# Kernel tuning notes

Measured on AMD Instinct MI355X. Metric: run time of the kernel, lower is better.

## Reference

```python
import jax, jax.numpy as jnp
import numpy as np

N = 4096
M = 1024
APPERTURE = 250
L1, L2, L3, PRED = 1024, 512, 128, 1
EPS = 1e-6


def _layer_norm(x, gamma, beta):
    # torch x.std(-1) is unbiased (ddof=1)
    mean = jnp.mean(x, axis=-1, keepdims=True)
    std = jnp.std(x, axis=-1, ddof=1, keepdims=True)
    return gamma * (x - mean) / (std + EPS) + beta


def _self_attention(x, Wq, Wk, Wv, Wo, band_mask):
    # x: [n, m]; Linear(bias=False) => x @ W.T
    K = x @ Wk.T
    Q = (x @ Wq.T) * 0.06
    V = x @ Wv.T
    logits = Q @ K.T                      # [n, n]
    logits = jnp.where(band_mask, logits, -jnp.inf)  # keep |i-j| < apperture
    att = jax.nn.softmax(logits, axis=-1)
    # original: y = (V^T @ att)^T == att^T @ V  (note the transpose!)
    y = att.T @ V
    return y @ Wo.T, att


def setup_inputs() -> dict:
    key = jax.random.key(0)
    ks = jax.random.split(key, 20)
    s = 0.02
    inp = {
        'x1': jax.random.normal(ks[0], (1, N, M), jnp.float32),
        'x2': jax.random.normal(ks[1], (1, N, M), jnp.float32),
        'x3': jax.random.normal(ks[2], (1, N, M), jnp.float32),
        'Wq': jax.random.normal(ks[3], (M, M), jnp.float32) * s,
        'Wk': jax.random.normal(ks[4], (M, M), jnp.float32) * s,
        'Wv': jax.random.normal(ks[5], (M, M), jnp.float32) * s,
        'Wo': jax.random.normal(ks[6], (M, M), jnp.float32) * s,
        'ka_w': jax.random.normal(ks[7], (L1, M), jnp.float32) * s,
        'ka_b': jnp.zeros((L1,), jnp.float32),
        'kb_w': jax.random.normal(ks[8], (L2, L1), jnp.float32) * s,
        'kb_b': jnp.zeros((L2,), jnp.float32),
        'kc_w': jax.random.normal(ks[9], (L3, L2), jnp.float32) * s,
        'kc_b': jnp.zeros((L3,), jnp.float32),
        'kd_w': jax.random.normal(ks[10], (PRED, L3), jnp.float32) * s,
        'kd_b': jnp.zeros((PRED,), jnp.float32),
        'g13': jnp.ones((M,), jnp.float32),
        'b13': jnp.zeros((M,), jnp.float32),
        'gkc': jnp.ones((L3,), jnp.float32),
        'bkc': jnp.zeros((L3,), jnp.float32),
        'seq_len': N,
    }
    return inp


def reference(x1, x2, x3, Wq, Wk, Wv, Wo, ka_w, ka_b, kb_w, kb_b, kc_w, kc_b,
              kd_w, kd_b, g13, b13, gkc, bkc, seq_len):
    x1 = x1.reshape(-1, x1.shape[2])
    x2 = x2.reshape(-1, x2.shape[2])
    x3 = x3.reshape(-1, x3.shape[2])
    n = x1.shape[0]
    idx = jnp.arange(n)
    band_mask = jnp.abs(idx[:, None] - idx[None, :]) < APPERTURE  # allowed

    y1, att1 = _self_attention(x1, Wq, Wk, Wv, Wo, band_mask)
    y2, _ = _self_attention(x2, Wq, Wk, Wv, Wo, band_mask)
    y3, _ = _self_attention(x3, Wq, Wk, Wv, Wo, band_mask)

    # residual + (dropout == identity in eval) + shared LayerNorm
    y1 = _layer_norm(y1 + x1, g13, b13)
    y2 = _layer_norm(y2 + x2, g13, b13)
    y3 = _layer_norm(y3 + x3, g13, b13)

    y = y1 + y2 + y3  # cmb == [1,1,1]
    y = y @ ka_w.T + ka_b
    y = y @ kb_w.T + kb_b
    y = jax.nn.relu(y @ kc_w.T + kc_b)
    y = _layer_norm(y, gkc, bkc)
    y = jax.nn.sigmoid(y @ kd_w.T + kd_b)
    return y.reshape(1, -1), att1
```

## Files before the change

kernel.cpp:

```cpp
#include <hip/hip_runtime.h>
#include <hip/hip_bf16.h>
#include <cstdint>
#include <cstddef>

#define NSEQ 4096
#define MDIM 1024

typedef __attribute__((ext_vector_type(8))) short short8;
typedef __attribute__((ext_vector_type(4))) float f32x4;
typedef __attribute__((ext_vector_type(2))) long long2v;
typedef __attribute__((ext_vector_type(8))) int int8v;
typedef __attribute__((ext_vector_type(4))) int int4v;

typedef const __attribute__((address_space(1))) void gvoid_t;
typedef __attribute__((address_space(3))) void lvoid_t;

__device__ __forceinline__ unsigned short f2b(float x) {
  union { float f; unsigned int u; } a; a.f = x;
  unsigned int r = (a.u + 0x7fffu + ((a.u >> 16) & 1u)) >> 16;
  return (unsigned short)r;
}
__device__ __forceinline__ float b2f(unsigned short u) {
  union { float f; unsigned int u32; } a; a.u32 = ((unsigned int)u) << 16;
  return a.f;
}
__device__ __forceinline__ unsigned char f2e4(float x) {
  return (unsigned char)(__builtin_amdgcn_cvt_pk_fp8_f32(x, x, 0, false) & 0xff);
}
__device__ __forceinline__ unsigned int f2e4x4(float a, float b, float c, float d) {
  unsigned int lo = __builtin_amdgcn_cvt_pk_fp8_f32(a, b, 0, false);
  return (unsigned int)__builtin_amdgcn_cvt_pk_fp8_f32(c, d, lo, true);
}

__device__ __forceinline__ int8v pack32(const unsigned char* p0,
                                        const unsigned char* p1) {
  int4v lo = *(const int4v*)p0;
  int4v hi = *(const int4v*)p1;
  int8v r;
  r[0] = lo[0]; r[1] = lo[1]; r[2] = lo[2]; r[3] = lo[3];
  r[4] = hi[0]; r[5] = hi[1]; r[6] = hi[2]; r[7] = hi[3];
  return r;
}

__global__ __launch_bounds__(256) void k_cvt_all(
    const float* __restrict__ s0, const float* __restrict__ s1,
    const float* __restrict__ s2, const float* __restrict__ s3,
    const float* __restrict__ s4, const float* __restrict__ s5,
    const float* __restrict__ s6,
    const float* __restrict__ xa, const float* __restrict__ xb,
    const float* __restrict__ xc,
    unsigned char* __restrict__ Wf8, unsigned short* __restrict__ Wmlp,
    unsigned char* __restrict__ Xdst) {
  int idx = blockIdx.x * 256 + threadIdx.x;
  if (idx < 1048576) {
    int seg = idx >> 18, local = idx & 262143;
    const float* src = (seg == 0) ? s0 : (seg == 1) ? s1 : (seg == 2) ? s2 : s3;
    float4 v = *(const float4*)(src + (size_t)local * 4);
    *(unsigned int*)(Wf8 + (size_t)idx * 4) =
        f2e4x4(v.x * 64.f, v.y * 64.f, v.z * 64.f, v.w * 64.f);
  } else if (idx < 1458176) {
    int i2 = idx - 1048576;
    const float* src; int local;
    if (i2 < 262144) { src = s4; local = i2; }
    else if (i2 < 393216) { src = s5; local = i2 - 262144; }
    else { src = s6; local = i2 - 393216; }
    float4 v = *(const float4*)(src + (size_t)local * 4);
    ushort4 o; o.x = f2b(v.x); o.y = f2b(v.y); o.z = f2b(v.z); o.w = f2b(v.w);
    *(ushort4*)(Wmlp + (size_t)i2 * 4) = o;
  } else {
    int i2 = idx - 1458176;
    int seg = i2 >> 20, local = i2 & 1048575;
    const float* src = (seg == 0) ? xa : (seg == 1) ? xb : xc;
    float4 v = *(const float4*)(src + (size_t)local * 4);
    *(unsigned int*)(Xdst + (size_t)i2 * 4) = f2e4x4(v.x, v.y, v.z, v.w);
  }
}

__global__ __launch_bounds__(256) void k_gemm(
    const unsigned char* __restrict__ A, int lda,
    const unsigned char* __restrict__ B, int ldb,
    void* __restrict__ Cout, void* __restrict__ Cout2, int ldc,
    int K, float alpha, int okind, int do_exp, int mode,
    const unsigned char* __restrict__ A1, const unsigned char* __restrict__ A2) {
  __shared__ unsigned char smem[4 * 128 * 128];
  int bx = blockIdx.x, by = blockIdx.y;
  const unsigned char* Ab;
  const unsigned char* Bb;
  void* Cdst = Cout;
  int k0 = 0, k1 = K, b_koff = 0;
  int ldce = ldc;
  int rbase, cbase;
  int ldae = lda, ldbe = ldb;
  if (mode == 0) {
    Ab = A + (size_t)by * 128 * lda;
    Bb = B + (size_t)bx * 128 * ldb;
    rbase = bx * 128; cbase = by * 128;
  } else if (mode == 3) {
    if (by < 16) {
      Ab = A + (size_t)by * 128 * lda;
      Bb = B + (size_t)bx * 128 * ldb;
      if (by >= 8) Cdst = Cout2;
      rbase = bx * 128; cbase = (by & 7) * 128;
    } else {
      Ab = B + (size_t)bx * 128 * ldb;
      Bb = A1 + (size_t)(by - 16) * 128 * 1024;
      Cdst = (void*)const_cast<unsigned char*>(A2);
      rbase = (by - 16) * 128; cbase = bx * 128;
      ldce = 3 * NSEQ;
    }
  } else if (mode == 1) {
    int s = bx >> 5, ti = bx & 31;
    int bt = ti + by - 2;
    if (bt < 0 || bt >= 32) return;
    Ab = A + (size_t)(s * 32 + bt) * 128 * lda;
    Bb = B + (size_t)bx * 128 * ldb;
    rbase = bx * 128; cbase = by * 128;
  } else {
    int s = bx >> 5, ti = bx & 31;
    Ab = A + (size_t)by * 128 * lda + s * NSEQ;
    const unsigned char* Bbase = (s == 0) ? B : ((s == 1) ? A1 : A2);
    Bb = Bbase + (size_t)ti * 128 * 640;
    ldbe = 640;
    int lo = ti - 2; if (lo < 0) lo = 0;
    int hi = ti + 3; if (hi > 32) hi = 32;
    k0 = lo * 128; k1 = hi * 128;
    b_koff = (ti - 2) * 128;
    rbase = bx * 128; cbase = by * 128;
  }

  const int t = threadIdx.x;
  const int l = t & 63;
  const int w = t >> 6;
  const int fr = l & 15;
  const int quad = l >> 4;
  const int wm = (w >> 1) * 64;
  const int wn = (w & 1) * 64;
  const int fq4 = quad * 4;

  int srow[4], scg[4], sloff[4];
#pragma unroll
  for (int j = 0; j < 4; j++) {
    srow[j] = w * 32 + j * 8 + (l >> 3);
    scg[j] = ((l & 7) - srow[j]) & 7;
    sloff[j] = (w * 32 + j * 8) * 128 + l * 16;
  }

  f32x4 acc[4][4];
#pragma unroll
  for (int m = 0; m < 4; m++)
#pragma unroll
    for (int n = 0; n < 4; n++) acc[m][n] = (f32x4){0.f, 0.f, 0.f, 0.f};

  const int c0 = quad * 2;
  const int nt = (k1 - k0) >> 7;

  {
    int kk = k0, kb = kk - b_koff;
#pragma unroll
    for (int j = 0; j < 4; j++)
      __builtin_amdgcn_global_load_lds(
          (gvoid_t*)(Ab + (size_t)srow[j] * ldae + kk + scg[j] * 16),
          (lvoid_t*)(smem + sloff[j]), 16, 0, 0);
#pragma unroll
    for (int j = 0; j < 4; j++)
      __builtin_amdgcn_global_load_lds(
          (gvoid_t*)(Bb + (size_t)srow[j] * ldbe + kb + scg[j] * 16),
          (lvoid_t*)(smem + 16384 + sloff[j]), 16, 0, 0);
  }

  for (int tt = 0; tt < nt; tt++) {
    __syncthreads();
    if (tt + 1 < nt) {
      int kk = k0 + (tt + 1) * 128, kb = kk - b_koff;
      unsigned char* Asn = smem + ((tt + 1) & 1) * 32768;
#pragma unroll
      for (int j = 0; j < 4; j++)
        __builtin_amdgcn_global_load_lds(
            (gvoid_t*)(Ab + (size_t)srow[j] * ldae + kk + scg[j] * 16),
            (lvoid_t*)(Asn + sloff[j]), 16, 0, 0);
#pragma unroll
      for (int j = 0; j < 4; j++)
        __builtin_amdgcn_global_load_lds(
            (gvoid_t*)(Bb + (size_t)srow[j] * ldbe + kb + scg[j] * 16),
            (lvoid_t*)(Asn + 16384 + sloff[j]), 16, 0, 0);
    }
    const unsigned char* Asc = smem + (tt & 1) * 32768;
    const unsigned char* Bsc = Asc + 16384;
    int8v a8[4], b8[4];
#pragma unroll
    for (int m = 0; m < 4; m++) {
      int r = wm + m * 16 + fr;
      int s0i = (c0 + r) & 7, s1i = (s0i + 1) & 7;
      a8[m] = pack32(Asc + r * 128 + s0i * 16, Asc + r * 128 + s1i * 16);
    }
#pragma unroll
    for (int n = 0; n < 4; n++) {
      int r = wn + n * 16 + fr;
      int s0i = (c0 + r) & 7, s1i = (s0i + 1) & 7;
      b8[n] = pack32(Bsc + r * 128 + s0i * 16, Bsc + r * 128 + s1i * 16);
    }
#pragma unroll
    for (int m = 0; m < 4; m++)
#pragma unroll
      for (int n = 0; n < 4; n++)
        acc[m][n] = __builtin_amdgcn_mfma_scale_f32_16x16x128_f8f6f4(
            a8[m], b8[n], acc[m][n], 0, 0, 0, 0x7F7F7F7F, 0, 0x7F7F7F7F);
  }

#pragma unroll
  for (int m = 0; m < 4; m++) {
#pragma unroll
    for (int n = 0; n < 4; n++) {
      int oc = cbase + wm + m * 16 + fq4;
      int orow = rbase + wn + n * 16 + fr;
      float v0 = acc[m][n][0] * alpha, v1 = acc[m][n][1] * alpha;
      float v2 = acc[m][n][2] * alpha, v3 = acc[m][n][3] * alpha;
      if (okind == 1) {
        if (do_exp) { v0 = __expf(v0); v1 = __expf(v1); v2 = __expf(v2); v3 = __expf(v3); }
        ushort4 o; o.x = f2b(v0); o.y = f2b(v1); o.z = f2b(v2); o.w = f2b(v3);
        *(uint2*)((unsigned short*)Cdst + (size_t)orow * ldce + oc) = *(uint2*)&o;
      } else if (okind == 2) {
        *(unsigned int*)((unsigned char*)Cdst + (size_t)orow * ldce + oc) =
            f2e4x4(v0, v1, v2, v3);
      } else {
        *(float4*)((float*)Cdst + (size_t)orow * ldce + oc) = make_float4(v0, v1, v2, v3);
      }
    }
  }
}

__global__ __launch_bounds__(256) void k_gemm64(
    const unsigned short* __restrict__ A, int lda,
    const unsigned short* __restrict__ B, int ldb,
    void* __restrict__ Cout, int ldc, int K,
    const float* __restrict__ bias, int relu, int out_bf16) {
  __shared__ unsigned short smem[4 * 64 * 64];
  int bx = blockIdx.x, by = blockIdx.y;
  const unsigned short* Ab = A + (size_t)by * 64 * lda;
  const unsigned short* Bb = B + (size_t)bx * 64 * ldb;
  int rbase = bx * 64, cbase = by * 64;

  const int t = threadIdx.x;
  const int l = t & 63;
  const int w = t >> 6;
  const int fr = l & 15;
  const int quad = l >> 4;
  const int wm = (w & 1) * 32;
  const int wn = (w >> 1) * 32;
  const int fq4 = quad * 4;

  int srow[2], scg[2], sloff[2];
#pragma unroll
  for (int j = 0; j < 2; j++) {
    srow[j] = w * 16 + j * 8 + (l >> 3);
    scg[j] = ((l & 7) - srow[j]) & 7;
    sloff[j] = (w * 16 + j * 8) * 64 + l * 8;
  }

  f32x4 acc[2][2];
#pragma unroll
  for (int m = 0; m < 2; m++)
#pragma unroll
    for (int n = 0; n < 2; n++) acc[m][n] = (f32x4){0.f, 0.f, 0.f, 0.f};

  const int nt = K >> 6;

#pragma unroll
  for (int j = 0; j < 2; j++)
    __builtin_amdgcn_global_load_lds(
        (gvoid_t*)(Ab + (size_t)srow[j] * lda + scg[j] * 8),
        (lvoid_t*)(smem + sloff[j]), 16, 0, 0);
#pragma unroll
  for (int j = 0; j < 2; j++)
    __builtin_amdgcn_global_load_lds(
        (gvoid_t*)(Bb + (size_t)srow[j] * ldb + scg[j] * 8),
        (lvoid_t*)(smem + 4096 + sloff[j]), 16, 0, 0);

  for (int tt = 0; tt < nt; tt++) {
    __syncthreads();
    if (tt + 1 < nt) {
      int kk = (tt + 1) * 64;
      unsigned short* Asn = smem + ((tt + 1) & 1) * 8192;
#pragma unroll
      for (int j = 0; j < 2; j++)
        __builtin_amdgcn_global_load_lds(
            (gvoid_t*)(Ab + (size_t)srow[j] * lda + kk + scg[j] * 8),
            (lvoid_t*)(Asn + sloff[j]), 16, 0, 0);
#pragma unroll
      for (int j = 0; j < 2; j++)
        __builtin_amdgcn_global_load_lds(
            (gvoid_t*)(Bb + (size_t)srow[j] * ldb + kk + scg[j] * 8),
            (lvoid_t*)(Asn + 4096 + sloff[j]), 16, 0, 0);
    }
    const unsigned short* Asc = smem + (tt & 1) * 8192;
    const unsigned short* Bsc = Asc + 4096;
#pragma unroll
    for (int s = 0; s < 2; s++) {
      short8 af[2], bf[2];
#pragma unroll
      for (int m = 0; m < 2; m++) {
        int r = wm + m * 16 + fr;
        int slot = (s * 4 + quad + r) & 7;
        af[m] = *(const short8*)(Asc + r * 64 + slot * 8);
      }
#pragma unroll
      for (int n = 0; n < 2; n++) {
        int r = wn + n * 16 + fr;
        int slot = (s * 4 + quad + r) & 7;
        bf[n] = *(const short8*)(Bsc + r * 64 + slot * 8);
      }
#pragma unroll
      for (int m = 0; m < 2; m++)
#pragma unroll
        for (int n = 0; n < 2; n++)
          acc[m][n] = __builtin_amdgcn_mfma_f32_16x16x32_bf16(af[m], bf[n], acc[m][n], 0, 0, 0);
    }
  }

#pragma unroll
  for (int m = 0; m < 2; m++) {
#pragma unroll
    for (int n = 0; n < 2; n++) {
      int oc = cbase + wm + m * 16 + fq4;
      int orow = rbase + wn + n * 16 + fr;
      float4 bv = bias ? *(const float4*)(bias + oc) : make_float4(0.f, 0.f, 0.f, 0.f);
      float v0 = acc[m][n][0] + bv.x, v1 = acc[m][n][1] + bv.y;
      float v2 = acc[m][n][2] + bv.z, v3 = acc[m][n][3] + bv.w;
      if (relu) {
        v0 = fmaxf(v0, 0.f); v1 = fmaxf(v1, 0.f);
        v2 = fmaxf(v2, 0.f); v3 = fmaxf(v3, 0.f);
      }
      if (out_bf16) {
        ushort4 o; o.x = f2b(v0); o.y = f2b(v1); o.z = f2b(v2); o.w = f2b(v3);
        *(uint2*)((unsigned short*)Cout + (size_t)orow * ldc + oc) = *(uint2*)&o;
      } else {
        *(float4*)((float*)Cout + (size_t)orow * ldc + oc) = make_float4(v0, v1, v2, v3);
      }
    }
  }
}

__global__ __launch_bounds__(256) void k_stats(const unsigned short* __restrict__ Eband,
                                               float* __restrict__ sums) {
  int ig = blockIdx.x * 4 + (threadIdx.x >> 6);
  int lane = threadIdx.x & 63;
  int i = ig & 4095;
  int ti = i >> 7;
  int cbase = (ti - 2) * 128;
  int jlo = i - 249; if (jlo < 0) jlo = 0;
  int jhi = i + 249; if (jhi > NSEQ - 1) jhi = NSEQ - 1;
  int clo = jlo - cbase, chi = jhi - cbase;
  const unsigned short* L = Eband + (size_t)ig * 640;
  float s = 0.f;
  for (int c = clo + lane; c <= chi; c += 64) s += b2f(L[c]);
  for (int off = 32; off; off >>= 1) s += __shfl_xor(s, off);
  if (lane == 0) sums[ig] = s;
}

__global__ __launch_bounds__(256) void k_build_attT(const unsigned short* __restrict__ Eband,
                                                    const float* __restrict__ sums,
                                                    unsigned char* __restrict__ t0,
                                                    unsigned char* __restrict__ t1,
                                                    unsigned char* __restrict__ t2) {
  int byy = blockIdx.y;
  int s = byy >> 5, ti = byy & 31;
  int tj = ti + (int)blockIdx.x - 2;
  if (tj < 0 || tj >= 32) return;
  unsigned char* dst = (s == 0) ? t0 : ((s == 1) ? t1 : t2);
  __shared__ unsigned char T[128][132];
  int t = threadIdx.x;
  int c0 = (ti - tj + 2) * 128;
  int colg = (t & 31) * 4;
  for (int jj = t >> 5; jj < 128; jj += 8) {
    int jg = s * NSEQ + tj * 128 + jj;
    float inv = 16.f / sums[jg];
    ushort4 v = *(const ushort4*)&Eband[(size_t)jg * 640 + c0 + colg];
    float vv[4] = {b2f(v.x), b2f(v.y), b2f(v.z), b2f(v.w)};
#pragma unroll
    for (int q = 0; q < 4; q++) {
      int i = ti * 128 + colg + q;
      int d = i - (tj * 128 + jj);
      float a = (d < 250 && d > -250) ? vv[q] * inv : 0.f;
      T[colg + q][jj] = f2e4(a);
    }
  }
  __syncthreads();
  int jb0 = (tj - ti + 2) * 128;
  for (int ii = t >> 5; ii < 128; ii += 8) {
    size_t o = (size_t)(ti * 128 + ii) * 640 + jb0 + colg;
    *(unsigned int*)(dst + o) = *(const unsigned int*)&T[ii][colg];
  }
}

__global__ __launch_bounds__(256) void k_write_att(const unsigned short* __restrict__ Eband,
                                                   const float* __restrict__ sums,
                                                   float* __restrict__ att) {
  int i = blockIdx.x;
  int ti = i >> 7, cbase = (ti - 2) * 128;
  int jlo = i - 249; if (jlo < 0) jlo = 0;
  int jhi = i + 249; if (jhi > NSEQ - 1) jhi = NSEQ - 1;
  float inv = 1.f / sums[i];
  const unsigned short* L = Eband + (size_t)i * 640;
  float* arow = att + (size_t)i * NSEQ;
  for (int j0 = threadIdx.x * 4; j0 < NSEQ; j0 += 1024) {
    float ov[4];
#pragma unroll
    for (int q = 0; q < 4; q++) {
      int j = j0 + q;
      ov[q] = (j >= jlo && j <= jhi) ? b2f(L[j - cbase]) * inv : 0.f;
    }
    *(float4*)(arow + j0) = make_float4(ov[0], ov[1], ov[2], ov[3]);
  }
}

__global__ __launch_bounds__(256) void k_ln3(const unsigned short* __restrict__ yo,
                                             const float* __restrict__ x1,
                                             const float* __restrict__ x2,
                                             const float* __restrict__ x3,
                                             const float* __restrict__ g,
                                             const float* __restrict__ b,
                                             unsigned short* __restrict__ ysum_b) {
  int i = blockIdx.x, t = threadIdx.x;
  int w = t >> 6, lane = t & 63;
  __shared__ float red[8];
  const float* xs[3] = {x1, x2, x3};
  float4 gg = *(const float4*)(g + t * 4);
  float4 bb = *(const float4*)(b + t * 4);
  float acc[4] = {0.f, 0.f, 0.f, 0.f};
  for (int s = 0; s < 3; s++) {
    ushort4 yv = *(const ushort4*)(yo + ((size_t)(s * NSEQ + i)) * MDIM + t * 4);
    float4 xx = *(const float4*)(xs[s] + (size_t)i * MDIM + t * 4);
    float v[4] = {b2f(yv.x) + xx.x, b2f(yv.y) + xx.y, b2f(yv.z) + xx.z, b2f(yv.w) + xx.w};
    float s1 = v[0] + v[1] + v[2] + v[3];
    float s2 = v[0]*v[0] + v[1]*v[1] + v[2]*v[2] + v[3]*v[3];
    for (int off = 32; off; off >>= 1) { s1 += __shfl_xor(s1, off); s2 += __shfl_xor(s2, off); }
    __syncthreads();
    if (lane == 0) { red[w] = s1; red[4 + w] = s2; }
    __syncthreads();
    float S1 = red[0] + red[1] + red[2] + red[3];
    float S2 = red[4] + red[5] + red[6] + red[7];
    float mean = S1 * (1.f / 1024.f);
    float var = (S2 - S1 * mean) * (1.f / 1023.f);
    float rstd = 1.f / (sqrtf(var) + 1e-6f);
    acc[0] += gg.x * (v[0] - mean) * rstd + bb.x;
    acc[1] += gg.y * (v[1] - mean) * rstd + bb.y;
    acc[2] += gg.z * (v[2] - mean) * rstd + bb.z;
    acc[3] += gg.w * (v[3] - mean) * rstd + bb.w;
  }
  ushort4 o;
  o.x = f2b(acc[0]); o.y = f2b(acc[1]); o.z = f2b(acc[2]); o.w = f2b(acc[3]);
  *(ushort4*)(ysum_b + (size_t)i * MDIM + t * 4) = o;
}

__global__ __launch_bounds__(128) void k_final(const float* __restrict__ h3,
                                               const float* __restrict__ g,
                                               const float* __restrict__ b,
                                               const float* __restrict__ kdw,
                                               const float* __restrict__ kdb,
                                               float* __restrict__ yout) {
  int i = blockIdx.x, t = threadIdx.x;
  float v = h3[(size_t)i * 128 + t];
  float s1 = v, s2 = v * v;
  for (int off = 32; off; off >>= 1) { s1 += __shfl_xor(s1, off); s2 += __shfl_xor(s2, off); }
  __shared__ float red[4];
  int w = t >> 6, lane = t & 63;
  if (lane == 0) { red[w] = s1; red[2 + w] = s2; }
  __syncthreads();
  float S1 = red[0] + red[1], S2 = red[2] + red[3];
  float mean = S1 * (1.f / 128.f);
  float var = (S2 - S1 * mean) * (1.f / 127.f);
  float rstd = 1.f / (sqrtf(var) + 1e-6f);
  float ln = g[t] * (v - mean) * rstd + b[t];
  float p = ln * kdw[t];
  for (int off = 32; off; off >>= 1) p += __shfl_xor(p, off);
  __syncthreads();
  if (lane == 0) red[w] = p;
  __syncthreads();
  if (t == 0) {
    float z = red[0] + red[1] + kdb[0];
    yout[i] = 1.f / (1.f + __expf(-z));
  }
}

extern "C" void kernel_launch(void* const* d_in, const int* in_sizes, int n_in,
                              void* d_out, int out_size, void* d_ws, size_t ws_size,
                              hipStream_t stream) {
  const float* x1 = (const float*)d_in[0];
  const float* x2 = (const float*)d_in[1];
  const float* x3 = (const float*)d_in[2];
  const float* Wq = (const float*)d_in[3];
  const float* Wk = (const float*)d_in[4];
  const float* Wv = (const float*)d_in[5];
  const float* Wo = (const float*)d_in[6];
  const float* ka_w = (const float*)d_in[7];
  const float* ka_b = (const float*)d_in[8];
  const float* kb_w = (const float*)d_in[9];
  const float* kb_b = (const float*)d_in[10];
  const float* kc_w = (const float*)d_in[11];
  const float* kc_b = (const float*)d_in[12];
  const float* kd_w = (const float*)d_in[13];
  const float* kd_b = (const float*)d_in[14];
  const float* g13 = (const float*)d_in[15];
  const float* b13 = (const float*)d_in[16];
  const float* gkc = (const float*)d_in[17];
  const float* bkc = (const float*)d_in[18];

  float* y_out = (float*)d_out;
  float* att_out = y_out + NSEQ;

  char* ws = (char*)d_ws;
  size_t off = 0;
  auto alloc = [&](size_t bytes) -> void* {
    void* p = ws + off;
    off += (bytes + 255) & ~(size_t)255;
    return p;
  };
  const size_t NM = (size_t)3 * NSEQ * MDIM;
  unsigned char* Wf = (unsigned char*)alloc(4 * 1048576);
  unsigned short* Wmlp = (unsigned short*)alloc((1048576 + 524288 + 65536) * 2);
  unsigned char* Xf = (unsigned char*)alloc(NM);
  unsigned char* Qf = (unsigned char*)alloc(NM);
  unsigned char* Kf = (unsigned char*)alloc(NM);
  unsigned char* VTf = (unsigned char*)alloc(NM);
  unsigned short* Eband = (unsigned short*)alloc((size_t)3 * NSEQ * 640 * 2);
  float* sums = (float*)alloc((size_t)3 * NSEQ * 4);
  unsigned char* aT0 = (unsigned char*)alloc((size_t)NSEQ * 640);
  unsigned char* aT1 = (unsigned char*)alloc((size_t)NSEQ * 640);
  unsigned char* aT2 = (unsigned char*)alloc((size_t)NSEQ * 640);
  unsigned char* Wv_f = Wf + 2097152;
  unsigned char* Wo_f = Wf + 3145728;
  unsigned short* ka_b16 = Wmlp;
  unsigned short* kb_b16 = Wmlp + 1048576;
  unsigned short* kc_b16 = Wmlp + 1572864;
  unsigned char* yb = Xf;
  unsigned short* yo = (unsigned short*)Qf;
  unsigned short* ysum_b = (unsigned short*)VTf;
  unsigned short* h1b = (unsigned short*)Xf;
  unsigned short* h2b = (unsigned short*)Qf;
  float* h3 = (float*)aT0;

  k_cvt_all<<<17984, 256, 0, stream>>>(Wq, Wk, Wv, Wo, ka_w, kb_w, kc_w,
                                       x1, x2, x3, Wf, Wmlp, Xf);

  k_gemm<<<dim3(96, 24), 256, 0, stream>>>(Wf, 1024, Xf, 1024, Qf, Kf, 1024,
                                           1024, 1.f / 64.f, 2, 0, 3, Wv_f, VTf);
  k_gemm<<<dim3(96, 5), 256, 0, stream>>>(Kf, 1024, Qf, 1024, Eband, nullptr, 640,
                                          1024, 0.06f, 1, 1, 1, nullptr, nullptr);
  k_stats<<<3072, 256, 0, stream>>>(Eband, sums);
  k_build_attT<<<dim3(5, 96), 256, 0, stream>>>(Eband, sums, aT0, aT1, aT2);
  k_gemm<<<dim3(96, 8), 256, 0, stream>>>(VTf, 3 * NSEQ, aT0, 640, yb, nullptr, 1024,
                                          NSEQ, 0.5f, 2, 0, 2, aT1, aT2);
  k_write_att<<<4096, 256, 0, stream>>>(Eband, sums, att_out);
  k_gemm<<<dim3(96, 8), 256, 0, stream>>>(Wo_f, 1024, yb, 1024, yo, nullptr, 1024,
                                          1024, 1.f / 512.f, 1, 0, 0, nullptr, nullptr);
  k_ln3<<<4096, 256, 0, stream>>>(yo, x1, x2, x3, g13, b13, ysum_b);

  k_gemm64<<<dim3(64, 16), 256, 0, stream>>>(ka_b16, 1024, ysum_b, 1024, h1b, 1024,
                                             1024, ka_b, 0, 1);
  k_gemm64<<<dim3(64, 8), 256, 0, stream>>>(kb_b16, 1024, h1b, 1024, h2b, 512,
                                            1024, kb_b, 0, 1);
  k_gemm64<<<dim3(64, 2), 256, 0, stream>>>(kc_b16, 512, h2b, 512, h3, 128,
                                            512, kc_b, 1, 0);
  k_final<<<4096, 128, 0, stream>>>(h3, gkc, bkc, kd_w, kd_b, y_out);
}
```

Before: 339.8 us.

## Fuse softmax row sums into band GEMM epilogue and single-buffer GEMM LDS

Removes the separate k_stats kernel by accumulating masked exp row sums in the band-logit GEMM epilogue, reduced with wave shuffles and atomicAdd into a sums buffer zeroed in the conversion kernel. This avoids rereading the bf16 band matrix. Separately, the GEMM shared-memory pipeline is reduced from double buffering to a single buffer with load-sync-compute per k-step. That halves LDS use but removes the overlap of global loads with MFMA work.

```diff
diff --git a/kernel.cpp b/kernel.cpp
--- a/kernel.cpp
+++ b/kernel.cpp
@@ -50,7 +50,7 @@
     const float* __restrict__ xa, const float* __restrict__ xb,
     const float* __restrict__ xc,
     unsigned char* __restrict__ Wf8, unsigned short* __restrict__ Wmlp,
-    unsigned char* __restrict__ Xdst) {
+    unsigned char* __restrict__ Xdst, float* __restrict__ sums) {
   int idx = blockIdx.x * 256 + threadIdx.x;
   if (idx < 1048576) {
     int seg = idx >> 18, local = idx & 262143;
@@ -67,12 +67,15 @@
     float4 v = *(const float4*)(src + (size_t)local * 4);
     ushort4 o; o.x = f2b(v.x); o.y = f2b(v.y); o.z = f2b(v.z); o.w = f2b(v.w);
     *(ushort4*)(Wmlp + (size_t)i2 * 4) = o;
-  } else {
+  } else if (idx < 4603904) {
     int i2 = idx - 1458176;
     int seg = i2 >> 20, local = i2 & 1048575;
     const float* src = (seg == 0) ? xa : (seg == 1) ? xb : xc;
     float4 v = *(const float4*)(src + (size_t)local * 4);
     *(unsigned int*)(Xdst + (size_t)i2 * 4) = f2e4x4(v.x, v.y, v.z, v.w);
+  } else {
+    int i3 = idx - 4603904;
+    *(float4*)(sums + (size_t)i3 * 4) = make_float4(0.f, 0.f, 0.f, 0.f);
   }
 }
 
@@ -81,8 +84,11 @@
     const unsigned char* __restrict__ B, int ldb,
     void* __restrict__ Cout, void* __restrict__ Cout2, int ldc,
     int K, float alpha, int okind, int do_exp, int mode,
-    const unsigned char* __restrict__ A1, const unsigned char* __restrict__ A2) {
-  __shared__ unsigned char smem[4 * 128 * 128];
+    const unsigned char* __restrict__ A1, const unsigned char* __restrict__ A2,
+    float* __restrict__ sums_out) {
+  __shared__ unsigned char smem[2 * 128 * 128];
+  unsigned char* As = smem;
+  unsigned char* Bs = smem + 128 * 128;
   int bx = blockIdx.x, by = blockIdx.y;
   const unsigned char* Ab;
   const unsigned char* Bb;
@@ -152,61 +158,45 @@
     for (int n = 0; n < 4; n++) acc[m][n] = (f32x4){0.f, 0.f, 0.f, 0.f};
 
   const int c0 = quad * 2;
-  const int nt = (k1 - k0) >> 7;
-
-  {
-    int kk = k0, kb = kk - b_koff;
+  for (int kk = k0; kk < k1; kk += 128) {
+    int kb = kk - b_koff;
+    __syncthreads();
 #pragma unroll
     for (int j = 0; j < 4; j++)
       __builtin_amdgcn_global_load_lds(
           (gvoid_t*)(Ab + (size_t)srow[j] * ldae + kk + scg[j] * 16),
-          (lvoid_t*)(smem + sloff[j]), 16, 0, 0);
+          (lvoid_t*)(As + sloff[j]), 16, 0, 0);
 #pragma unroll
     for (int j = 0; j < 4; j++)
       __builtin_amdgcn_global_load_lds(
           (gvoid_t*)(Bb + (size_t)srow[j] * ldbe + kb + scg[j] * 16),
-          (lvoid_t*)(smem + 16384 + sloff[j]), 16, 0, 0);
-  }
-
-  for (int tt = 0; tt < nt; tt++) {
+          (lvoid_t*)(Bs + sloff[j]), 16, 0, 0);
     __syncthreads();
-    if (tt + 1 < nt) {
-      int kk = k0 + (tt + 1) * 128, kb = kk - b_koff;
-      unsigned char* Asn = smem + ((tt + 1) & 1) * 32768;
-#pragma unroll
-      for (int j = 0; j < 4; j++)
-        __builtin_amdgcn_global_load_lds(
-            (gvoid_t*)(Ab + (size_t)srow[j] * ldae + kk + scg[j] * 16),
-            (lvoid_t*)(Asn + sloff[j]), 16, 0, 0);
-#pragma unroll
-      for (int j = 0; j < 4; j++)
-        __builtin_amdgcn_global_load_lds(
-            (gvoid_t*)(Bb + (size_t)srow[j] * ldbe + kb + scg[j] * 16),
-            (lvoid_t*)(Asn + 16384 + sloff[j]), 16, 0, 0);
-    }
-    const unsigned char* Asc = smem + (tt & 1) * 32768;
-    const unsigned char* Bsc = Asc + 16384;
-    int8v a8[4], b8[4];
-#pragma unroll
-    for (int m = 0; m < 4; m++) {
-      int r = wm + m * 16 + fr;
-      int s0i = (c0 + r) & 7, s1i = (s0i + 1) & 7;
-      a8[m] = pack32(Asc + r * 128 + s0i * 16, Asc + r * 128 + s1i * 16);
-    }
-#pragma unroll
-    for (int n = 0; n < 4; n++) {
-      int r = wn + n * 16 + fr;
-      int s0i = (c0 + r) & 7, s1i = (s0i + 1) & 7;
-      b8[n] = pack32(Bsc + r * 128 + s0i * 16, Bsc + r * 128 + s1i * 16);
-    }
-#pragma unroll
-    for (int m = 0; m < 4; m++)
-#pragma unroll
-      for (int n = 0; n < 4; n++)
-        acc[m][n] = __builtin_amdgcn_mfma_scale_f32_16x16x128_f8f6f4(
-            a8[m], b8[n], acc[m][n], 0, 0, 0, 0x7F7F7F7F, 0, 0x7F7F7F7F);
-  }
-
+    {
+      int8v a8[4], b8[4];
+#pragma unroll
+      for (int m = 0; m < 4; m++) {
+        int r = wm + m * 16 + fr;
+        int s0i = (c0 + r) & 7, s1i = (s0i + 1) & 7;
+        a8[m] = pack32(As + r * 128 + s0i * 16, As + r * 128 + s1i * 16);
+      }
+#pragma unroll
+      for (int n = 0; n < 4; n++) {
+        int r = wn + n * 16 + fr;
+        int s0i = (c0 + r) & 7, s1i = (s0i + 1) & 7;
+        b8[n] = pack32(Bs + r * 128 + s0i * 16, Bs + r * 128 + s1i * 16);
+      }
+#pragma unroll
+      for (int m = 0; m < 4; m++)
+#pragma unroll
+        for (int n = 0; n < 4; n++)
+          acc[m][n] = __builtin_amdgcn_mfma_scale_f32_16x16x128_f8f6f4(
+              a8[m], b8[n], acc[m][n], 0, 0, 0, 0x7F7F7F7F, 0, 0x7F7F7F7F);
+    }
+  }
+
+  float rowsum[4] = {0.f, 0.f, 0.f, 0.f};
+  const int jb = (mode == 1) ? ((bx & 31) - 2) * 128 : 0;
 #pragma unroll
   for (int m = 0; m < 4; m++) {
 #pragma unroll
@@ -216,7 +206,16 @@
       float v0 = acc[m][n][0] * alpha, v1 = acc[m][n][1] * alpha;
       float v2 = acc[m][n][2] * alpha, v3 = acc[m][n][3] * alpha;
       if (okind == 1) {
-        if (do_exp) { v0 = __expf(v0); v1 = __expf(v1); v2 = __expf(v2); v3 = __expf(v3); }
+        if (do_exp) {
+          v0 = __expf(v0); v1 = __expf(v1); v2 = __expf(v2); v3 = __expf(v3);
+          if (mode == 1) {
+            int d0 = (orow & 4095) - (jb + oc);
+            rowsum[n] += ((unsigned)(d0 + 249) < 499u ? v0 : 0.f)
+                       + ((unsigned)(d0 + 248) < 499u ? v1 : 0.f)
+                       + ((unsigned)(d0 + 247) < 499u ? v2 : 0.f)
+                       + ((unsigned)(d0 + 246) < 499u ? v3 : 0.f);
+          }
+        }
         ushort4 o; o.x = f2b(v0); o.y = f2b(v1); o.z = f2b(v2); o.w = f2b(v3);
         *(uint2*)((unsigned short*)Cdst + (size_t)orow * ldce + oc) = *(uint2*)&o;
       } else if (okind == 2) {
@@ -224,6 +223,18 @@
             f2e4x4(v0, v1, v2, v3);
       } else {
         *(float4*)((float*)Cdst + (size_t)orow * ldce + oc) = make_float4(v0, v1, v2, v3);
+      }
+    }
+  }
+  if (mode == 1 && do_exp) {
+#pragma unroll
+    for (int n = 0; n < 4; n++) {
+      float sv = rowsum[n];
+      sv += __shfl_xor(sv, 16);
+      sv += __shfl_xor(sv, 32);
+      if (quad == 0) {
+        int orow = rbase + wn + n * 16 + fr;
+        atomicAdd(sums_out + orow, sv);
       }
     }
   }
@@ -338,23 +349,6 @@
       }
     }
   }
-}
-
-__global__ __launch_bounds__(256) void k_stats(const unsigned short* __restrict__ Eband,
-                                               float* __restrict__ sums) {
-  int ig = blockIdx.x * 4 + (threadIdx.x >> 6);
-  int lane = threadIdx.x & 63;
-  int i = ig & 4095;
-  int ti = i >> 7;
-  int cbase = (ti - 2) * 128;
-  int jlo = i - 249; if (jlo < 0) jlo = 0;
-  int jhi = i + 249; if (jhi > NSEQ - 1) jhi = NSEQ - 1;
-  int clo = jlo - cbase, chi = jhi - cbase;
-  const unsigned short* L = Eband + (size_t)ig * 640;
-  float s = 0.f;
-  for (int c = clo + lane; c <= chi; c += 64) s += b2f(L[c]);
-  for (int off = 32; off; off >>= 1) s += __shfl_xor(s, off);
-  if (lane == 0) sums[ig] = s;
 }
 
 __global__ __launch_bounds__(256) void k_build_attT(const unsigned short* __restrict__ Eband,
@@ -539,20 +533,19 @@
   unsigned short* h2b = (unsigned short*)Qf;
   float* h3 = (float*)aT0;
 
-  k_cvt_all<<<17984, 256, 0, stream>>>(Wq, Wk, Wv, Wo, ka_w, kb_w, kc_w,
-                                       x1, x2, x3, Wf, Wmlp, Xf);
+  k_cvt_all<<<17996, 256, 0, stream>>>(Wq, Wk, Wv, Wo, ka_w, kb_w, kc_w,
+                                       x1, x2, x3, Wf, Wmlp, Xf, sums);
 
   k_gemm<<<dim3(96, 24), 256, 0, stream>>>(Wf, 1024, Xf, 1024, Qf, Kf, 1024,
-                                           1024, 1.f / 64.f, 2, 0, 3, Wv_f, VTf);
+                                           1024, 1.f / 64.f, 2, 0, 3, Wv_f, VTf, nullptr);
   k_gemm<<<dim3(96, 5), 256, 0, stream>>>(Kf, 1024, Qf, 1024, Eband, nullptr, 640,
-                                          1024, 0.06f, 1, 1, 1, nullptr, nullptr);
-  k_stats<<<3072, 256, 0, stream>>>(Eband, sums);
+                                          1024, 0.06f, 1, 1, 1, nullptr, nullptr, sums);
   k_build_attT<<<dim3(5, 96), 256, 0, stream>>>(Eband, sums, aT0, aT1, aT2);
   k_gemm<<<dim3(96, 8), 256, 0, stream>>>(VTf, 3 * NSEQ, aT0, 640, yb, nullptr, 1024,
-                                          NSEQ, 0.5f, 2, 0, 2, aT1, aT2);
+                                          NSEQ, 0.5f, 2, 0, 2, aT1, aT2, nullptr);
   k_write_att<<<4096, 256, 0, stream>>>(Eband, sums, att_out);
   k_gemm<<<dim3(96, 8), 256, 0, stream>>>(Wo_f, 1024, yb, 1024, yo, nullptr, 1024,
-                                          1024, 1.f / 512.f, 1, 0, 0, nullptr, nullptr);
+                                          1024, 1.f / 512.f, 1, 0, 0, nullptr, nullptr, nullptr);
   k_ln3<<<4096, 256, 0, stream>>>(yo, x1, x2, x3, g13, b13, ysum_b);
 
   k_gemm64<<<dim3(64, 16), 256, 0, stream>>>(ka_b16, 1024, ysum_b, 1024, h1b, 1024,
```

Result: no change. 344.0 us (+1.2%).
